# Performance work log

Hardware: AMD Instinct MI355X
Metric: run time of the kernel (lower is better)

Reference implementation:

```python
import jax, jax.numpy as jnp
import numpy as np

B_, L, D_MODEL = 2, 2048, 1024
EXPAND, D_INNER, D_STATE, DT_RANK, D_CONV = 2, 2048, 16, 64, 4
DT_MIN, DT_MAX = 0.001, 0.1


def setup_inputs() -> dict:
    key = jax.random.key(0)
    ks = jax.random.split(key, 8)
    s = lambda fan: 1.0 / np.sqrt(fan)
    # S4D-real style init for A: A = -exp(A_log), A_log = log(1..n) repeated over d_inner
    A0 = jnp.broadcast_to(jnp.arange(1, D_STATE + 1, dtype=jnp.float32), (D_INNER, D_STATE))
    return {
        "x": jax.random.normal(ks[0], (B_, L, D_MODEL), jnp.float32),
        "W_in": jax.random.normal(ks[1], (D_MODEL, 2 * D_INNER), jnp.float32) * s(D_MODEL),
        "conv_k": jax.random.normal(ks[2], (D_CONV, D_INNER // EXPAND, D_INNER), jnp.float32) * s(D_CONV * D_INNER // EXPAND),
        "conv_b": jnp.zeros((D_INNER,), jnp.float32),
        "W_x": jax.random.normal(ks[3], (D_INNER, DT_RANK + 2 * D_STATE), jnp.float32) * s(D_INNER),
        "W_dt": jax.random.normal(ks[4], (DT_RANK, D_INNER), jnp.float32) * s(DT_RANK),
        "b_dt": jnp.zeros((D_INNER,), jnp.float32),
        "A_log": jnp.log(A0),
        "D": jnp.ones((D_INNER,), jnp.float32),
        "W_out": jax.random.normal(ks[5], (D_INNER, D_MODEL), jnp.float32) * s(D_INNER),
    }


def reference(x, W_in, conv_k, conv_b, W_x, W_dt, b_dt, A_log, D, W_out):
    # in_proj -> split into ssm branch and gating residual branch
    xz = x @ W_in                                   # (b, l, 2*d_inner)
    xs, res = jnp.split(xz, 2, axis=-1)
    # causal grouped conv1d (feature_group_count = expand)
    xc = jax.lax.conv_general_dilated(
        xs, conv_k, window_strides=(1,), padding=[(D_CONV - 1, 0)],
        dimension_numbers=("NWC", "WIO", "NWC"), feature_group_count=EXPAND,
    ) + conv_b
    u = jax.nn.silu(xc)                             # (b, l, d_inner)
    # x_proj -> delta(low-rank), B, C
    dbc = u @ W_x                                   # (b, l, dt_rank + 2n)
    dt_raw = dbc[..., :DT_RANK]
    Bm = dbc[..., DT_RANK:DT_RANK + D_STATE]        # (b, l, n)
    Cm = dbc[..., DT_RANK + D_STATE:]               # (b, l, n)
    delta = jax.nn.softplus(dt_raw @ W_dt + b_dt)   # (b, l, d_inner)
    delta = jnp.clip(delta, DT_MIN, DT_MAX)
    A = -jnp.exp(A_log)                             # (d_inner, n)
    dA = jnp.exp(delta[..., None] * A)              # (b, l, d_inner, n)
    dBu = delta[..., None] * u[..., None] * Bm[:, :, None, :]  # (b, l, d_inner, n)

    def step(h, inp):
        dA_t, dBu_t, C_t = inp                      # (b,d,n),(b,d,n),(b,n)
        h = dA_t * h + dBu_t
        y_t = jnp.einsum('bdn,bn->bd', h, C_t)
        return h, y_t

    h0 = jnp.zeros((x.shape[0], D_INNER, D_STATE), dA.dtype)
    _, y = jax.lax.scan(step, h0, (dA.transpose(1, 0, 2, 3), dBu.transpose(1, 0, 2, 3), Cm.transpose(1, 0, 2)))
    y = y.transpose(1, 0, 2) + u * D                # (b, l, d_inner)
    out = (y * jax.nn.silu(res)) @ W_out            # (b, l, d_model)
    return out
```

## Files before the change

kernel.cpp:

```cpp
#include <hip/hip_runtime.h>
#include <math.h>


typedef unsigned short ushort_t;
typedef __bf16 bf16x8 __attribute__((ext_vector_type(8)));
typedef float floatx4 __attribute__((ext_vector_type(4)));

#define LDS_STRIDE 40

__device__ __forceinline__ float silu_f(float x) { return x / (1.0f + __expf(-x)); }

__device__ __forceinline__ unsigned short f2bf(float f) {
    unsigned u = __float_as_uint(f);
    unsigned r = u + 0x7fffu + ((u >> 16) & 1u);
    return (unsigned short)(r >> 16);
}
__device__ __forceinline__ float bf2f(unsigned short h) {
    return __uint_as_float(((unsigned)h) << 16);
}

__global__ __launch_bounds__(256) void prep_all(
    const float* __restrict__ x, const float* __restrict__ W_in,
    const float* __restrict__ conv_k, const float* __restrict__ W_out,
    const float* __restrict__ W_x,
    ushort_t* __restrict__ x_h, ushort_t* __restrict__ x_l,
    ushort_t* __restrict__ WinT_h, ushort_t* __restrict__ convkT_h,
    ushort_t* __restrict__ WoutT_h, ushort_t* __restrict__ WxT_h,
    ushort_t* __restrict__ XSP_h)
{
    __shared__ float ts[32][33];
    const int bid = blockIdx.x;
    const int t = threadIdx.x;
    if (bid < 4096) {
        const size_t i4 = ((size_t)bid * 256 + t) * 4;
        float4 v = *(const float4*)&x[i4];
        unsigned short h0 = f2bf(v.x), h1 = f2bf(v.y), h2 = f2bf(v.z), h3 = f2bf(v.w);
        unsigned short l0 = f2bf(v.x - bf2f(h0)), l1 = f2bf(v.y - bf2f(h1));
        unsigned short l2 = f2bf(v.z - bf2f(h2)), l3 = f2bf(v.w - bf2f(h3));
        *(uint2*)&x_h[i4] = make_uint2((unsigned)h0 | ((unsigned)h1 << 16),
                                       (unsigned)h2 | ((unsigned)h3 << 16));
        *(uint2*)&x_l[i4] = make_uint2((unsigned)l0 | ((unsigned)l1 << 16),
                                       (unsigned)l2 | ((unsigned)l3 << 16));
        return;
    }
    if (bid >= 18432 && bid < 19456) {
        const int idx = (bid - 18432) * 256 + t;
        const int r = idx >> 11, k = idx & 2047;
        float v = (r < 96) ? W_x[(size_t)k * 96 + r] : 0.f;
        WxT_h[idx] = f2bf(v);
        return;
    }
    if (bid >= 19456) {
        const int idx = (bid - 19456) * 256 + t;
        const int b = idx / 6144, rem = idx % 6144;
        const int lp = rem >> 11, c = rem & 2047;
        XSP_h[((size_t)b * 2051 + lp) * 2048 + c] = 0;
        return;
    }
    const float* src; int R, C; ushort_t* dst; int bx, by;
    if (bid < 8192)       { src = W_in;   R = 1024; C = 4096; dst = WinT_h;
                            int l = bid - 4096;  bx = l & 127; by = l >> 7; }
    else if (bid < 16384) { src = conv_k; R = 4096; C = 2048; dst = convkT_h;
                            int l = bid - 8192;  bx = l & 63;  by = l >> 6; }
    else                  { src = W_out;  R = 2048; C = 1024; dst = WoutT_h;
                            int l = bid - 16384; bx = l & 31;  by = l >> 5; }
    const int tx = t & 31, ty = t >> 5;
    const int r0 = by * 32, c0 = bx * 32;
    #pragma unroll
    for (int j = 0; j < 4; ++j)
        ts[ty + j * 8][tx] = src[(size_t)(r0 + ty + j * 8) * C + c0 + tx];
    __syncthreads();
    #pragma unroll
    for (int j = 0; j < 4; ++j)
        dst[(size_t)(c0 + ty + j * 8) * R + r0 + tx] = f2bf(ts[tx][ty + j * 8]);
}

template<int MODE, int BX>
__global__ __launch_bounds__(256) void gemm2(
    const ushort_t* __restrict__ Ah, const ushort_t* __restrict__ Al,
    const ushort_t* __restrict__ Bh, int Kfull,
    float* __restrict__ Cf, ushort_t* __restrict__ Oh)
{
    __shared__ __align__(16) ushort_t As_h[128 * LDS_STRIDE];
    __shared__ __align__(16) ushort_t As_l[128 * LDS_STRIDE];
    __shared__ __align__(16) ushort_t Bs_h[128 * LDS_STRIDE];
    const int t = threadIdx.x;
    int bx, by;
    if (MODE == 2) { bx = blockIdx.x; by = blockIdx.y; }
    else {
        const int lin = blockIdx.x, xcd = lin & 7, s = lin >> 3;
        by = xcd + 8 * (s / BX);
        bx = s % BX;
    }
    const int m0 = by * 128;
    const int n0 = (MODE == 2) ? 0 : bx * 128;
    const int kbeg = (MODE == 2) ? bx * 512 : 0;
    const int kend = (MODE == 2) ? kbeg + 512 : Kfull;
    const int lane = t & 63, wave = t >> 6;
    const int wm = (wave >> 1) * 64, wn = (wave & 1) * 64;
    const int m16 = lane & 15, q = lane >> 4;
    const int r_0 = t >> 2, cc_0 = (t & 3) * 8;
    const int r_1 = (t + 256) >> 2, cc_1 = ((t + 256) & 3) * 8;

    uint4 pa0h = *(const uint4*)&Ah[(size_t)(m0 + r_0) * Kfull + kbeg + cc_0];
    uint4 pa1h = *(const uint4*)&Ah[(size_t)(m0 + r_1) * Kfull + kbeg + cc_1];
    uint4 pa0l = *(const uint4*)&Al[(size_t)(m0 + r_0) * Kfull + kbeg + cc_0];
    uint4 pa1l = *(const uint4*)&Al[(size_t)(m0 + r_1) * Kfull + kbeg + cc_1];
    uint4 pb0  = *(const uint4*)&Bh[(size_t)(n0 + r_0) * Kfull + kbeg + cc_0];
    uint4 pb1  = *(const uint4*)&Bh[(size_t)(n0 + r_1) * Kfull + kbeg + cc_1];

    floatx4 acc[4][4];
    const floatx4 zz = {0.f, 0.f, 0.f, 0.f};
    #pragma unroll
    for (int i = 0; i < 4; ++i)
        #pragma unroll
        for (int j = 0; j < 4; ++j) acc[i][j] = zz;

    for (int k0 = kbeg; k0 < kend; k0 += 32) {
        *(uint4*)&As_h[r_0 * LDS_STRIDE + cc_0] = pa0h;
        *(uint4*)&As_h[r_1 * LDS_STRIDE + cc_1] = pa1h;
        *(uint4*)&As_l[r_0 * LDS_STRIDE + cc_0] = pa0l;
        *(uint4*)&As_l[r_1 * LDS_STRIDE + cc_1] = pa1l;
        *(uint4*)&Bs_h[r_0 * LDS_STRIDE + cc_0] = pb0;
        *(uint4*)&Bs_h[r_1 * LDS_STRIDE + cc_1] = pb1;
        __syncthreads();
        if (k0 + 32 < kend) {
            const int kn = k0 + 32;
            pa0h = *(const uint4*)&Ah[(size_t)(m0 + r_0) * Kfull + kn + cc_0];
            pa1h = *(const uint4*)&Ah[(size_t)(m0 + r_1) * Kfull + kn + cc_1];
            pa0l = *(const uint4*)&Al[(size_t)(m0 + r_0) * Kfull + kn + cc_0];
            pa1l = *(const uint4*)&Al[(size_t)(m0 + r_1) * Kfull + kn + cc_1];
            pb0  = *(const uint4*)&Bh[(size_t)(n0 + r_0) * Kfull + kn + cc_0];
            pb1  = *(const uint4*)&Bh[(size_t)(n0 + r_1) * Kfull + kn + cc_1];
        }
        bf16x8 ah[4], al[4], bh[4];
        #pragma unroll
        for (int i = 0; i < 4; ++i) {
            const int off = (wm + i * 16 + m16) * LDS_STRIDE + q * 8;
            ah[i] = *(const bf16x8*)&As_h[off];
            al[i] = *(const bf16x8*)&As_l[off];
        }
        #pragma unroll
        for (int j = 0; j < 4; ++j)
            bh[j] = *(const bf16x8*)&Bs_h[(wn + j * 16 + m16) * LDS_STRIDE + q * 8];
        #pragma unroll
        for (int i = 0; i < 4; ++i)
            #pragma unroll
            for (int j = 0; j < 4; ++j) {
                acc[i][j] = __builtin_amdgcn_mfma_f32_16x16x32_bf16(ah[i], bh[j], acc[i][j], 0, 0, 0);
                acc[i][j] = __builtin_amdgcn_mfma_f32_16x16x32_bf16(al[i], bh[j], acc[i][j], 0, 0, 0);
            }
        __syncthreads();
    }

    float* Cp = (MODE == 2) ? (Cf + (size_t)bx * 393216) : Cf;
    #pragma unroll
    for (int i = 0; i < 4; ++i) {
        const int row_b = m0 + wm + i * 16 + q * 4;
        #pragma unroll
        for (int j = 0; j < 4; ++j) {
            const int col = n0 + wn + j * 16 + m16;
            #pragma unroll
            for (int rr = 0; rr < 4; ++rr) {
                const int row = row_b + rr;
                const float v = acc[i][j][rr];
                if (MODE == 0) {
                    if (n0 < 2048) {
                        const int b = row >> 11, l = row & 2047;
                        Oh[((size_t)b * 2051 + l + 3) * 2048 + col] = f2bf(v);
                    } else {
                        Cp[(size_t)row * 2048 + (col - 2048)] = v;
                    }
                } else if (MODE == 1) {
                    Cp[(size_t)row * 1024 + col] = v;
                } else {
                    if (col < 96) Cp[(size_t)row * 96 + col] = v;
                }
            }
        }
    }
}

__global__ __launch_bounds__(256) void conv2(
    const ushort_t* __restrict__ Xh, const ushort_t* __restrict__ Bh,
    const float* __restrict__ bias,
    ushort_t* __restrict__ Uh, ushort_t* __restrict__ Ul)
{
    __shared__ __align__(16) ushort_t As_h[128 * LDS_STRIDE];
    __shared__ __align__(16) ushort_t Bs_h[128 * LDS_STRIDE];
    const int t = threadIdx.x;
    const int lin = blockIdx.x, xcd = lin & 7, s = lin >> 3;
    const int by = xcd + 8 * (s / 16);
    const int bxp = s % 16;
    const int m0 = by * 128, n0 = bxp * 128;
    const int g1024 = (n0 >= 1024) ? 1024 : 0;
    const int lane = t & 63, wave = t >> 6;
    const int wm = (wave >> 1) * 64, wn = (wave & 1) * 64;
    const int m16 = lane & 15, q = lane >> 4;
    const int r_0 = t >> 2, cc_0 = (t & 3) * 8;
    const int r_1 = (t + 256) >> 2, cc_1 = ((t + 256) & 3) * 8;
    const int p_0 = m0 + r_0, b_0 = p_0 >> 11, l_0 = p_0 & 2047;
    const int p_1 = m0 + r_1, b_1 = p_1 >> 11, l_1 = p_1 & 2047;

    auto aA = [&](int bb, int ll, int k0, int cc) -> size_t {
        const int w = k0 >> 10;
        const int i = (k0 & 1023) + cc;
        return ((size_t)bb * 2051 + ll + w) * 2048 + g1024 + i;
    };

    uint4 pa0 = *(const uint4*)&Xh[aA(b_0, l_0, 0, cc_0)];
    uint4 pa1 = *(const uint4*)&Xh[aA(b_1, l_1, 0, cc_1)];
    uint4 pb0 = *(const uint4*)&Bh[(size_t)(n0 + r_0) * 4096 + cc_0];
    uint4 pb1 = *(const uint4*)&Bh[(size_t)(n0 + r_1) * 4096 + cc_1];

    floatx4 acc[4][4];
    const floatx4 zz = {0.f, 0.f, 0.f, 0.f};
    #pragma unroll
    for (int i = 0; i < 4; ++i)
        #pragma unroll
        for (int j = 0; j < 4; ++j) acc[i][j] = zz;

    for (int k0 = 0; k0 < 4096; k0 += 32) {
        *(uint4*)&As_h[r_0 * LDS_STRIDE + cc_0] = pa0;
        *(uint4*)&As_h[r_1 * LDS_STRIDE + cc_1] = pa1;
        *(uint4*)&Bs_h[r_0 * LDS_STRIDE + cc_0] = pb0;
        *(uint4*)&Bs_h[r_1 * LDS_STRIDE + cc_1] = pb1;
        __syncthreads();
        if (k0 + 32 < 4096) {
            const int kn = k0 + 32;
            pa0 = *(const uint4*)&Xh[aA(b_0, l_0, kn, cc_0)];
            pa1 = *(const uint4*)&Xh[aA(b_1, l_1, kn, cc_1)];
            pb0 = *(const uint4*)&Bh[(size_t)(n0 + r_0) * 4096 + kn + cc_0];
            pb1 = *(const uint4*)&Bh[(size_t)(n0 + r_1) * 4096 + kn + cc_1];
        }
        bf16x8 ah[4], bh[4];
        #pragma unroll
        for (int i = 0; i < 4; ++i)
            ah[i] = *(const bf16x8*)&As_h[(wm + i * 16 + m16) * LDS_STRIDE + q * 8];
        #pragma unroll
        for (int j = 0; j < 4; ++j)
            bh[j] = *(const bf16x8*)&Bs_h[(wn + j * 16 + m16) * LDS_STRIDE + q * 8];
        #pragma unroll
        for (int i = 0; i < 4; ++i)
            #pragma unroll
            for (int j = 0; j < 4; ++j)
                acc[i][j] = __builtin_amdgcn_mfma_f32_16x16x32_bf16(ah[i], bh[j], acc[i][j], 0, 0, 0);
        __syncthreads();
    }

    #pragma unroll
    for (int i = 0; i < 4; ++i) {
        const int row_b = m0 + wm + i * 16 + q * 4;
        #pragma unroll
        for (int j = 0; j < 4; ++j) {
            const int col = n0 + wn + j * 16 + m16;
            const float bz = bias[col];
            #pragma unroll
            for (int rr = 0; rr < 4; ++rr) {
                const int row = row_b + rr;
                const float v = silu_f(acc[i][j][rr] + bz);
                const size_t a = (size_t)row * 2048 + col;
                const unsigned short h = f2bf(v);
                Uh[a] = h;
                Ul[a] = f2bf(v - bf2f(h));
            }
        }
    }
}

__global__ __launch_bounds__(256) void dbc_reduce(
    const float* __restrict__ DBCP, float* __restrict__ DBC)
{
    const int i = blockIdx.x * 256 + threadIdx.x;
    DBC[i] = (DBCP[i] + DBCP[393216 + i]) + (DBCP[786432 + i] + DBCP[1179648 + i]);
}

__global__ __launch_bounds__(256) void delta_kernel(
    const float* __restrict__ DBC, const float* __restrict__ W_dt,
    const float* __restrict__ b_dt, float* __restrict__ DELTA)
{
    const int n  = blockIdx.x * 256 + threadIdx.x;
    const int p0 = blockIdx.y * 16;
    const int t  = threadIdx.x;
    __shared__ float dt_s[16][64];
    #pragma unroll
    for (int j = 0; j < 4; ++j) {
        const int lin = j * 256 + t;
        const int r = lin >> 6, k = lin & 63;
        dt_s[r][k] = DBC[(size_t)(p0 + r) * 96 + k];
    }
    __syncthreads();
    float acc[16];
    const float bz = b_dt[n];
    #pragma unroll
    for (int r = 0; r < 16; ++r) acc[r] = bz;
    for (int k = 0; k < 64; ++k) {
        const float wv = W_dt[(size_t)k * 2048 + n];
        #pragma unroll
        for (int r = 0; r < 16; ++r) acc[r] += dt_s[r][k] * wv;
    }
    #pragma unroll
    for (int r = 0; r < 16; ++r) {
        float a = acc[r];
        float sp = (a > 20.f) ? a : log1pf(expf(a));
        sp = fminf(fmaxf(sp, 0.001f), 0.1f);
        DELTA[(size_t)(p0 + r) * 2048 + n] = sp;
    }
}

__global__ __launch_bounds__(256) void scan_p1(
    const float* __restrict__ DELTA,
    const ushort_t* __restrict__ Uh, const ushort_t* __restrict__ Ul,
    const float* __restrict__ DBC, const float* __restrict__ A_log,
    float* __restrict__ HEND, float* __restrict__ APROD)
{
    const int t = threadIdx.x;
    const int d = blockIdx.x * 256 + t;
    const int c = blockIdx.y;
    const int b = blockIdx.z;
    const int p0 = b * 2048 + c * 32;
    __shared__ float Bs[32][16];
    for (int lin = t; lin < 512; lin += 256) {
        const int s = lin >> 4, n = lin & 15;
        Bs[s][n] = DBC[(size_t)(p0 + s) * 96 + 64 + n];
    }
    __syncthreads();
    float Af[16];
    *(float4*)&Af[0]  = *(const float4*)&A_log[(size_t)d * 16 + 0];
    *(float4*)&Af[4]  = *(const float4*)&A_log[(size_t)d * 16 + 4];
    *(float4*)&Af[8]  = *(const float4*)&A_log[(size_t)d * 16 + 8];
    *(float4*)&Af[12] = *(const float4*)&A_log[(size_t)d * 16 + 12];
    #pragma unroll
    for (int n = 0; n < 16; ++n) Af[n] = -__expf(Af[n]);

    float h[16] = {};
    float sd = 0.f;
    for (int s = 0; s < 32; ++s) {
        const size_t ix = (size_t)(p0 + s) * 2048 + d;
        const float dv = DELTA[ix];
        const float uv = bf2f(Uh[ix]) + bf2f(Ul[ix]);
        const float du = dv * uv;
        sd += dv;
        #pragma unroll
        for (int n = 0; n < 16; ++n)
            h[n] = __expf(dv * Af[n]) * h[n] + du * Bs[s][n];
    }
    const size_t base = (size_t)c * 65536 + (size_t)b * 2048 + d;
    #pragma unroll
    for (int n = 0; n < 16; ++n) {
        HEND[base + (size_t)n * 4096]  = h[n];
        APROD[base + (size_t)n * 4096] = __expf(Af[n] * sd);
    }
}

__global__ __launch_bounds__(256) void scan_p2(
    const float* __restrict__ HEND, const float* __restrict__ APROD,
    float* __restrict__ HINIT)
{
    const int g = blockIdx.x * 256 + threadIdx.x;
    float h = 0.f;
    for (int c = 0; c < 64; ++c) {
        HINIT[(size_t)c * 65536 + g] = h;
        h = APROD[(size_t)c * 65536 + g] * h + HEND[(size_t)c * 65536 + g];
    }
}

__global__ __launch_bounds__(256) void scan_p3(
    const float* __restrict__ DELTA,
    const ushort_t* __restrict__ Uh, const ushort_t* __restrict__ Ul,
    const float* __restrict__ DBC, const float* __restrict__ RES,
    const float* __restrict__ A_log, const float* __restrict__ Dp,
    const float* __restrict__ HINIT,
    ushort_t* __restrict__ Gh, ushort_t* __restrict__ Gl)
{
    const int t = threadIdx.x;
    const int d = blockIdx.x * 256 + t;
    const int c = blockIdx.y;
    const int b = blockIdx.z;
    const int p0 = b * 2048 + c * 32;
    __shared__ float Bs[32][16];
    __shared__ float Cs[32][16];
    for (int lin = t; lin < 512; lin += 256) {
        const int s = lin >> 4, n = lin & 15;
        Bs[s][n] = DBC[(size_t)(p0 + s) * 96 + 64 + n];
        Cs[s][n] = DBC[(size_t)(p0 + s) * 96 + 80 + n];
    }
    __syncthreads();
    float Af[16];
    *(float4*)&Af[0]  = *(const float4*)&A_log[(size_t)d * 16 + 0];
    *(float4*)&Af[4]  = *(const float4*)&A_log[(size_t)d * 16 + 4];
    *(float4*)&Af[8]  = *(const float4*)&A_log[(size_t)d * 16 + 8];
    *(float4*)&Af[12] = *(const float4*)&A_log[(size_t)d * 16 + 12];
    #pragma unroll
    for (int n = 0; n < 16; ++n) Af[n] = -__expf(Af[n]);

    const size_t base = (size_t)c * 65536 + (size_t)b * 2048 + d;
    float h[16];
    #pragma unroll
    for (int n = 0; n < 16; ++n) h[n] = HINIT[base + (size_t)n * 4096];
    const float Dd = Dp[d];

    for (int s = 0; s < 32; ++s) {
        const int p = p0 + s;
        const size_t ix = (size_t)p * 2048 + d;
        const float dv = DELTA[ix];
        const float uv = bf2f(Uh[ix]) + bf2f(Ul[ix]);
        const float du = dv * uv;
        float y = 0.f;
        #pragma unroll
        for (int n = 0; n < 16; ++n) {
            h[n] = __expf(dv * Af[n]) * h[n] + du * Bs[s][n];
            y += h[n] * Cs[s][n];
        }
        const float resv = RES[ix];
        const float gv = (y + uv * Dd) * silu_f(resv);
        const unsigned short gh = f2bf(gv);
        Gh[ix] = gh;
        Gl[ix] = f2bf(gv - bf2f(gh));
    }
}

extern "C" void kernel_launch(void* const* d_in, const int* in_sizes, int n_in,
                              void* d_out, int out_size, void* d_ws, size_t ws_size,
                              hipStream_t stream) {
    const float* x      = (const float*)d_in[0];
    const float* W_in   = (const float*)d_in[1];
    const float* conv_k = (const float*)d_in[2];
    const float* conv_b = (const float*)d_in[3];
    const float* W_x    = (const float*)d_in[4];
    const float* W_dt   = (const float*)d_in[5];
    const float* b_dt   = (const float*)d_in[6];
    const float* A_log  = (const float*)d_in[7];
    const float* Dv     = (const float*)d_in[8];
    const float* W_out  = (const float*)d_in[9];
    float* out = (float*)d_out;

    char* base = (char*)d_ws;
    float*    RES      = (float*)(base);
    ushort_t* Uh       = (ushort_t*)(base + 33554432);
    ushort_t* Ul       = (ushort_t*)(base + 50331648);
    float*    DELTA    = (float*)(base + 67108864);
    ushort_t* XSP_h    = (ushort_t*)(base + 100663296);
    float*    HEND     = (float*)(base + 100663296);
    float*    APROD    = (float*)(base + 117440512);
    ushort_t* x_h      = (ushort_t*)(base + 134266880);
    ushort_t* x_l      = (ushort_t*)(base + 142655488);
    ushort_t* convkT_h = (ushort_t*)(base + 151044096);
    ushort_t* G_h      = (ushort_t*)(base + 134266880);
    ushort_t* G_l      = (ushort_t*)(base + 151044096);
    ushort_t* WinT_h   = (ushort_t*)(base + 167821312);
    ushort_t* WoutT_h  = (ushort_t*)(base + 176209920);
    ushort_t* WxT_h    = (ushort_t*)(base + 180404224);
    float*    DBCP     = (float*)(base + 180928512);
    float*    DBC      = (float*)(base + 187219968);
    float*    HINIT    = (float*)(base + 188792832);

    prep_all<<<19504, 256, 0, stream>>>(x, W_in, conv_k, W_out, W_x,
                                        x_h, x_l, WinT_h, convkT_h, WoutT_h,
                                        WxT_h, XSP_h);
    gemm2<0, 32><<<1024, 256, 0, stream>>>(x_h, x_l, WinT_h, 1024, RES, XSP_h);
    conv2<<<512, 256, 0, stream>>>(XSP_h, convkT_h, conv_b, Uh, Ul);
    gemm2<2, 4><<<dim3(4, 32), 256, 0, stream>>>(Uh, Ul, WxT_h, 2048, DBCP, nullptr);
    dbc_reduce<<<1536, 256, 0, stream>>>(DBCP, DBC);
    delta_kernel<<<dim3(8, 256), 256, 0, stream>>>(DBC, W_dt, b_dt, DELTA);
    scan_p1<<<dim3(8, 64, 2), 256, 0, stream>>>(DELTA, Uh, Ul, DBC, A_log, HEND, APROD);
    scan_p2<<<256, 256, 0, stream>>>(HEND, APROD, HINIT);
    scan_p3<<<dim3(8, 64, 2), 256, 0, stream>>>(DELTA, Uh, Ul, DBC, RES, A_log, Dv,
                                                HINIT, G_h, G_l);
    gemm2<1, 8><<<256, 256, 0, stream>>>(G_h, G_l, WoutT_h, 2048, out, nullptr);
}
```

Before: 515.2 us.

## Interleave bf16 hi/lo split into packed words and restructure scan carry storage

Activations stored as separate bf16 high and low arrays (x, u, gated output) now go into a single 32-bit word per element holding both halves. Each element then costs one load or store instead of two. The GEMM unpacks these words into separate hi/lo LDS tiles. The scan chunk carries move to a d-major layout with float4 accesses, and scan_p2 recomputes the decay product from a stored delta sum instead of reading a precomputed APROD array. Block-to-tile swizzles for the GEMM and conv are also changed, at the cost of extra unpacking ALU work and wider 32-byte-per-row A loads in the GEMM.

```diff
diff --git a/kernel.cpp b/kernel.cpp
--- a/kernel.cpp
+++ b/kernel.cpp
@@ -3,6 +3,7 @@
 
 
 typedef unsigned short ushort_t;
+typedef unsigned int uint_t;
 typedef __bf16 bf16x8 __attribute__((ext_vector_type(8)));
 typedef float floatx4 __attribute__((ext_vector_type(4)));
 
@@ -18,12 +19,26 @@
 __device__ __forceinline__ float bf2f(unsigned short h) {
     return __uint_as_float(((unsigned)h) << 16);
 }
+__device__ __forceinline__ uint_t packhl(float v) {
+    const unsigned short h = f2bf(v);
+    const unsigned short l = f2bf(v - bf2f(h));
+    return (uint_t)h | ((uint_t)l << 16);
+}
+__device__ __forceinline__ float unpack_sum(uint_t pk) {
+    return __uint_as_float(pk << 16) + __uint_as_float(pk & 0xffff0000u);
+}
+__device__ __forceinline__ void unpack8(uint4 w0, uint4 w1, uint4& H, uint4& L) {
+    H.x = (w0.x & 0xffffu) | (w0.y << 16);  L.x = (w0.x >> 16) | (w0.y & 0xffff0000u);
+    H.y = (w0.z & 0xffffu) | (w0.w << 16);  L.y = (w0.z >> 16) | (w0.w & 0xffff0000u);
+    H.z = (w1.x & 0xffffu) | (w1.y << 16);  L.z = (w1.x >> 16) | (w1.y & 0xffff0000u);
+    H.w = (w1.z & 0xffffu) | (w1.w << 16);  L.w = (w1.z >> 16) | (w1.w & 0xffff0000u);
+}
 
 __global__ __launch_bounds__(256) void prep_all(
     const float* __restrict__ x, const float* __restrict__ W_in,
     const float* __restrict__ conv_k, const float* __restrict__ W_out,
     const float* __restrict__ W_x,
-    ushort_t* __restrict__ x_h, ushort_t* __restrict__ x_l,
+    uint_t* __restrict__ xpk,
     ushort_t* __restrict__ WinT_h, ushort_t* __restrict__ convkT_h,
     ushort_t* __restrict__ WoutT_h, ushort_t* __restrict__ WxT_h,
     ushort_t* __restrict__ XSP_h)
@@ -34,13 +49,9 @@
     if (bid < 4096) {
         const size_t i4 = ((size_t)bid * 256 + t) * 4;
         float4 v = *(const float4*)&x[i4];
-        unsigned short h0 = f2bf(v.x), h1 = f2bf(v.y), h2 = f2bf(v.z), h3 = f2bf(v.w);
-        unsigned short l0 = f2bf(v.x - bf2f(h0)), l1 = f2bf(v.y - bf2f(h1));
-        unsigned short l2 = f2bf(v.z - bf2f(h2)), l3 = f2bf(v.w - bf2f(h3));
-        *(uint2*)&x_h[i4] = make_uint2((unsigned)h0 | ((unsigned)h1 << 16),
-                                       (unsigned)h2 | ((unsigned)h3 << 16));
-        *(uint2*)&x_l[i4] = make_uint2((unsigned)l0 | ((unsigned)l1 << 16),
-                                       (unsigned)l2 | ((unsigned)l3 << 16));
+        uint4 pk;
+        pk.x = packhl(v.x); pk.y = packhl(v.y); pk.z = packhl(v.z); pk.w = packhl(v.w);
+        *(uint4*)&xpk[i4] = pk;
         return;
     }
     if (bid >= 18432 && bid < 19456) {
@@ -75,10 +86,9 @@
         dst[(size_t)(c0 + ty + j * 8) * R + r0 + tx] = f2bf(ts[tx][ty + j * 8]);
 }
 
-template<int MODE, int BX>
+template<int MODE>
 __global__ __launch_bounds__(256) void gemm2(
-    const ushort_t* __restrict__ Ah, const ushort_t* __restrict__ Al,
-    const ushort_t* __restrict__ Bh, int Kfull,
+    const uint_t* __restrict__ Apk, const ushort_t* __restrict__ Bh, int Kfull,
     float* __restrict__ Cf, ushort_t* __restrict__ Oh)
 {
     __shared__ __align__(16) ushort_t As_h[128 * LDS_STRIDE];
@@ -89,8 +99,8 @@
     if (MODE == 2) { bx = blockIdx.x; by = blockIdx.y; }
     else {
         const int lin = blockIdx.x, xcd = lin & 7, s = lin >> 3;
-        by = xcd + 8 * (s / BX);
-        bx = s % BX;
+        bx = s >> 2;
+        by = xcd * 4 + (s & 3);
     }
     const int m0 = by * 128;
     const int n0 = (MODE == 2) ? 0 : bx * 128;
@@ -102,12 +112,12 @@
     const int r_0 = t >> 2, cc_0 = (t & 3) * 8;
     const int r_1 = (t + 256) >> 2, cc_1 = ((t + 256) & 3) * 8;
 
-    uint4 pa0h = *(const uint4*)&Ah[(size_t)(m0 + r_0) * Kfull + kbeg + cc_0];
-    uint4 pa1h = *(const uint4*)&Ah[(size_t)(m0 + r_1) * Kfull + kbeg + cc_1];
-    uint4 pa0l = *(const uint4*)&Al[(size_t)(m0 + r_0) * Kfull + kbeg + cc_0];
-    uint4 pa1l = *(const uint4*)&Al[(size_t)(m0 + r_1) * Kfull + kbeg + cc_1];
-    uint4 pb0  = *(const uint4*)&Bh[(size_t)(n0 + r_0) * Kfull + kbeg + cc_0];
-    uint4 pb1  = *(const uint4*)&Bh[(size_t)(n0 + r_1) * Kfull + kbeg + cc_1];
+    uint4 a00 = *(const uint4*)&Apk[(size_t)(m0 + r_0) * Kfull + kbeg + cc_0];
+    uint4 a01 = *(const uint4*)&Apk[(size_t)(m0 + r_0) * Kfull + kbeg + cc_0 + 4];
+    uint4 a10 = *(const uint4*)&Apk[(size_t)(m0 + r_1) * Kfull + kbeg + cc_1];
+    uint4 a11 = *(const uint4*)&Apk[(size_t)(m0 + r_1) * Kfull + kbeg + cc_1 + 4];
+    uint4 pb0 = *(const uint4*)&Bh[(size_t)(n0 + r_0) * Kfull + kbeg + cc_0];
+    uint4 pb1 = *(const uint4*)&Bh[(size_t)(n0 + r_1) * Kfull + kbeg + cc_1];
 
     floatx4 acc[4][4];
     const floatx4 zz = {0.f, 0.f, 0.f, 0.f};
@@ -117,21 +127,24 @@
         for (int j = 0; j < 4; ++j) acc[i][j] = zz;
 
     for (int k0 = kbeg; k0 < kend; k0 += 32) {
-        *(uint4*)&As_h[r_0 * LDS_STRIDE + cc_0] = pa0h;
-        *(uint4*)&As_h[r_1 * LDS_STRIDE + cc_1] = pa1h;
-        *(uint4*)&As_l[r_0 * LDS_STRIDE + cc_0] = pa0l;
-        *(uint4*)&As_l[r_1 * LDS_STRIDE + cc_1] = pa1l;
+        uint4 H, L;
+        unpack8(a00, a01, H, L);
+        *(uint4*)&As_h[r_0 * LDS_STRIDE + cc_0] = H;
+        *(uint4*)&As_l[r_0 * LDS_STRIDE + cc_0] = L;
+        unpack8(a10, a11, H, L);
+        *(uint4*)&As_h[r_1 * LDS_STRIDE + cc_1] = H;
+        *(uint4*)&As_l[r_1 * LDS_STRIDE + cc_1] = L;
         *(uint4*)&Bs_h[r_0 * LDS_STRIDE + cc_0] = pb0;
         *(uint4*)&Bs_h[r_1 * LDS_STRIDE + cc_1] = pb1;
         __syncthreads();
         if (k0 + 32 < kend) {
             const int kn = k0 + 32;
-            pa0h = *(const uint4*)&Ah[(size_t)(m0 + r_0) * Kfull + kn + cc_0];
-            pa1h = *(const uint4*)&Ah[(size_t)(m0 + r_1) * Kfull + kn + cc_1];
-            pa0l = *(const uint4*)&Al[(size_t)(m0 + r_0) * Kfull + kn + cc_0];
-            pa1l = *(const uint4*)&Al[(size_t)(m0 + r_1) * Kfull + kn + cc_1];
-            pb0  = *(const uint4*)&Bh[(size_t)(n0 + r_0) * Kfull + kn + cc_0];
-            pb1  = *(const uint4*)&Bh[(size_t)(n0 + r_1) * Kfull + kn + cc_1];
+            a00 = *(const uint4*)&Apk[(size_t)(m0 + r_0) * Kfull + kn + cc_0];
+            a01 = *(const uint4*)&Apk[(size_t)(m0 + r_0) * Kfull + kn + cc_0 + 4];
+            a10 = *(const uint4*)&Apk[(size_t)(m0 + r_1) * Kfull + kn + cc_1];
+            a11 = *(const uint4*)&Apk[(size_t)(m0 + r_1) * Kfull + kn + cc_1 + 4];
+            pb0 = *(const uint4*)&Bh[(size_t)(n0 + r_0) * Kfull + kn + cc_0];
+            pb1 = *(const uint4*)&Bh[(size_t)(n0 + r_1) * Kfull + kn + cc_1];
         }
         bf16x8 ah[4], al[4], bh[4];
         #pragma unroll
@@ -183,15 +196,15 @@
 
 __global__ __launch_bounds__(256) void conv2(
     const ushort_t* __restrict__ Xh, const ushort_t* __restrict__ Bh,
-    const float* __restrict__ bias,
-    ushort_t* __restrict__ Uh, ushort_t* __restrict__ Ul)
+    const float* __restrict__ bias, uint_t* __restrict__ Upk)
 {
     __shared__ __align__(16) ushort_t As_h[128 * LDS_STRIDE];
     __shared__ __align__(16) ushort_t Bs_h[128 * LDS_STRIDE];
     const int t = threadIdx.x;
     const int lin = blockIdx.x, xcd = lin & 7, s = lin >> 3;
-    const int by = xcd + 8 * (s / 16);
-    const int bxp = s % 16;
+    const int sweep = s >> 5, r = s & 31;
+    const int bxp = r >> 1;
+    const int by = xcd * 4 + ((sweep << 1) | (r & 1));
     const int m0 = by * 128, n0 = bxp * 128;
     const int g1024 = (n0 >= 1024) ? 1024 : 0;
     const int lane = t & 63, wave = t >> 6;
@@ -259,10 +272,7 @@
             for (int rr = 0; rr < 4; ++rr) {
                 const int row = row_b + rr;
                 const float v = silu_f(acc[i][j][rr] + bz);
-                const size_t a = (size_t)row * 2048 + col;
-                const unsigned short h = f2bf(v);
-                Uh[a] = h;
-                Ul[a] = f2bf(v - bf2f(h));
+                Upk[(size_t)row * 2048 + col] = packhl(v);
             }
         }
     }
@@ -309,10 +319,9 @@
 }
 
 __global__ __launch_bounds__(256) void scan_p1(
-    const float* __restrict__ DELTA,
-    const ushort_t* __restrict__ Uh, const ushort_t* __restrict__ Ul,
+    const float* __restrict__ DELTA, const uint_t* __restrict__ Upk,
     const float* __restrict__ DBC, const float* __restrict__ A_log,
-    float* __restrict__ HEND, float* __restrict__ APROD)
+    float* __restrict__ HEND, float* __restrict__ SD)
 {
     const int t = threadIdx.x;
     const int d = blockIdx.x * 256 + t;
@@ -338,40 +347,43 @@
     for (int s = 0; s < 32; ++s) {
         const size_t ix = (size_t)(p0 + s) * 2048 + d;
         const float dv = DELTA[ix];
-        const float uv = bf2f(Uh[ix]) + bf2f(Ul[ix]);
+        const float uv = unpack_sum(Upk[ix]);
         const float du = dv * uv;
         sd += dv;
         #pragma unroll
         for (int n = 0; n < 16; ++n)
             h[n] = __expf(dv * Af[n]) * h[n] + du * Bs[s][n];
     }
-    const size_t base = (size_t)c * 65536 + (size_t)b * 2048 + d;
-    #pragma unroll
-    for (int n = 0; n < 16; ++n) {
-        HEND[base + (size_t)n * 4096]  = h[n];
-        APROD[base + (size_t)n * 4096] = __expf(Af[n] * sd);
-    }
+    const size_t hb = (((size_t)c * 2 + b) * 2048 + d) * 16;
+    *(float4*)&HEND[hb + 0]  = *(float4*)&h[0];
+    *(float4*)&HEND[hb + 4]  = *(float4*)&h[4];
+    *(float4*)&HEND[hb + 8]  = *(float4*)&h[8];
+    *(float4*)&HEND[hb + 12] = *(float4*)&h[12];
+    SD[((size_t)c * 2 + b) * 2048 + d] = sd;
 }
 
 __global__ __launch_bounds__(256) void scan_p2(
-    const float* __restrict__ HEND, const float* __restrict__ APROD,
-    float* __restrict__ HINIT)
+    const float* __restrict__ HEND, const float* __restrict__ SD,
+    const float* __restrict__ A_log, float* __restrict__ HINIT)
 {
     const int g = blockIdx.x * 256 + threadIdx.x;
+    const int n = g & 15, d = (g >> 4) & 2047, b = (g >> 15) & 1;
+    const float Af = -__expf(A_log[(size_t)d * 16 + n]);
     float h = 0.f;
+    #pragma unroll 8
     for (int c = 0; c < 64; ++c) {
-        HINIT[(size_t)c * 65536 + g] = h;
-        h = APROD[(size_t)c * 65536 + g] * h + HEND[(size_t)c * 65536 + g];
+        const size_t cb = (size_t)c * 2 + b;
+        const size_t idx = (cb * 2048 + d) * 16 + n;
+        HINIT[idx] = h;
+        h = __expf(Af * SD[cb * 2048 + d]) * h + HEND[idx];
     }
 }
 
 __global__ __launch_bounds__(256) void scan_p3(
-    const float* __restrict__ DELTA,
-    const ushort_t* __restrict__ Uh, const ushort_t* __restrict__ Ul,
+    const float* __restrict__ DELTA, const uint_t* __restrict__ Upk,
     const float* __restrict__ DBC, const float* __restrict__ RES,
     const float* __restrict__ A_log, const float* __restrict__ Dp,
-    const float* __restrict__ HINIT,
-    ushort_t* __restrict__ Gh, ushort_t* __restrict__ Gl)
+    const float* __restrict__ HINIT, uint_t* __restrict__ Gpk)
 {
     const int t = threadIdx.x;
     const int d = blockIdx.x * 256 + t;
@@ -394,17 +406,19 @@
     #pragma unroll
     for (int n = 0; n < 16; ++n) Af[n] = -__expf(Af[n]);
 
-    const size_t base = (size_t)c * 65536 + (size_t)b * 2048 + d;
+    const size_t hb = (((size_t)c * 2 + b) * 2048 + d) * 16;
     float h[16];
-    #pragma unroll
-    for (int n = 0; n < 16; ++n) h[n] = HINIT[base + (size_t)n * 4096];
+    *(float4*)&h[0]  = *(const float4*)&HINIT[hb + 0];
+    *(float4*)&h[4]  = *(const float4*)&HINIT[hb + 4];
+    *(float4*)&h[8]  = *(const float4*)&HINIT[hb + 8];
+    *(float4*)&h[12] = *(const float4*)&HINIT[hb + 12];
     const float Dd = Dp[d];
 
     for (int s = 0; s < 32; ++s) {
         const int p = p0 + s;
         const size_t ix = (size_t)p * 2048 + d;
         const float dv = DELTA[ix];
-        const float uv = bf2f(Uh[ix]) + bf2f(Ul[ix]);
+        const float uv = unpack_sum(Upk[ix]);
         const float du = dv * uv;
         float y = 0.f;
         #pragma unroll
@@ -414,9 +428,7 @@
         }
         const float resv = RES[ix];
         const float gv = (y + uv * Dd) * silu_f(resv);
-        const unsigned short gh = f2bf(gv);
-        Gh[ix] = gh;
-        Gl[ix] = f2bf(gv - bf2f(gh));
+        Gpk[ix] = packhl(gv);
     }
 }
 
@@ -437,35 +449,32 @@
 
     char* base = (char*)d_ws;
     float*    RES      = (float*)(base);
-    ushort_t* Uh       = (ushort_t*)(base + 33554432);
-    ushort_t* Ul       = (ushort_t*)(base + 50331648);
+    uint_t*   Upk      = (uint_t*)(base + 33554432);
     float*    DELTA    = (float*)(base + 67108864);
     ushort_t* XSP_h    = (ushort_t*)(base + 100663296);
     float*    HEND     = (float*)(base + 100663296);
-    float*    APROD    = (float*)(base + 117440512);
-    ushort_t* x_h      = (ushort_t*)(base + 134266880);
-    ushort_t* x_l      = (ushort_t*)(base + 142655488);
-    ushort_t* convkT_h = (ushort_t*)(base + 151044096);
-    ushort_t* G_h      = (ushort_t*)(base + 134266880);
-    ushort_t* G_l      = (ushort_t*)(base + 151044096);
-    ushort_t* WinT_h   = (ushort_t*)(base + 167821312);
-    ushort_t* WoutT_h  = (ushort_t*)(base + 176209920);
-    ushort_t* WxT_h    = (ushort_t*)(base + 180404224);
-    float*    DBCP     = (float*)(base + 180928512);
-    float*    DBC      = (float*)(base + 187219968);
-    float*    HINIT    = (float*)(base + 188792832);
+    uint_t*   xpk      = (uint_t*)(base + 117465088);
+    ushort_t* convkT_h = (ushort_t*)(base + 134242304);
+    uint_t*   Gpk      = (uint_t*)(base + 117465088);
+    ushort_t* WinT_h   = (ushort_t*)(base + 151019520);
+    ushort_t* WoutT_h  = (ushort_t*)(base + 159408128);
+    ushort_t* WxT_h    = (ushort_t*)(base + 163602432);
+    float*    DBCP     = (float*)(base + 164126720);
+    float*    DBC      = (float*)(base + 170418176);
+    float*    SD       = (float*)(base + 171991040);
+    float*    HINIT    = (float*)(base + 173039616);
 
     prep_all<<<19504, 256, 0, stream>>>(x, W_in, conv_k, W_out, W_x,
-                                        x_h, x_l, WinT_h, convkT_h, WoutT_h,
+                                        xpk, WinT_h, convkT_h, WoutT_h,
                                         WxT_h, XSP_h);
-    gemm2<0, 32><<<1024, 256, 0, stream>>>(x_h, x_l, WinT_h, 1024, RES, XSP_h);
-    conv2<<<512, 256, 0, stream>>>(XSP_h, convkT_h, conv_b, Uh, Ul);
-    gemm2<2, 4><<<dim3(4, 32), 256, 0, stream>>>(Uh, Ul, WxT_h, 2048, DBCP, nullptr);
+    gemm2<0><<<1024, 256, 0, stream>>>(xpk, WinT_h, 1024, RES, XSP_h);
+    conv2<<<512, 256, 0, stream>>>(XSP_h, convkT_h, conv_b, Upk);
+    gemm2<2><<<dim3(4, 32), 256, 0, stream>>>(Upk, WxT_h, 2048, DBCP, nullptr);
     dbc_reduce<<<1536, 256, 0, stream>>>(DBCP, DBC);
     delta_kernel<<<dim3(8, 256), 256, 0, stream>>>(DBC, W_dt, b_dt, DELTA);
-    scan_p1<<<dim3(8, 64, 2), 256, 0, stream>>>(DELTA, Uh, Ul, DBC, A_log, HEND, APROD);
-    scan_p2<<<256, 256, 0, stream>>>(HEND, APROD, HINIT);
-    scan_p3<<<dim3(8, 64, 2), 256, 0, stream>>>(DELTA, Uh, Ul, DBC, RES, A_log, Dv,
-                                                HINIT, G_h, G_l);
-    gemm2<1, 8><<<256, 256, 0, stream>>>(G_h, G_l, WoutT_h, 2048, out, nullptr);
-}
+    scan_p1<<<dim3(8, 64, 2), 256, 0, stream>>>(DELTA, Upk, DBC, A_log, HEND, SD);
+    scan_p2<<<256, 256, 0, stream>>>(HEND, SD, A_log, HINIT);
+    scan_p3<<<dim3(8, 64, 2), 256, 0, stream>>>(DELTA, Upk, DBC, RES, A_log, Dv,
+                                                HINIT, Gpk);
+    gemm2<1><<<256, 256, 0, stream>>>(Gpk, WoutT_h, 2048, out, nullptr);
+}
```

New measurement: 494.3 us. -4.1%, faster.
